# Kernel optimization log

Hardware: AMD Instinct MI355X
Metric: run time of the kernel (lower is better)

Reference implementation:

```python
import jax, jax.numpy as jnp
import numpy as np

KS = 4                       # kernel cells per axis
NCELL = KS ** 3              # 64 filter cells
K_NEIGH = 64                 # max neighbors kept per query point
EXTENT = float(40 * 6 * 0.025)   # radius_scale*6*particle_radius = 6.0
DT = 0.1
PI = float(np.pi)
BIG = 1e30
EPS = 1e-8
N_FLUID, N_BOX, BOX_L = 3000, 1500, 17.5
CH = [32, 64, 64, 64, 3]
C0 = 3

_OFFS = jnp.array([[i, j, l] for i in (0, 1) for j in (0, 1) for l in (0, 1)], dtype=jnp.int32)  # [8,3]


def _ball_to_cube(u):
    # Volume-preserving unit-ball -> unit-cube map (Open3D: sphere->cylinder->cube).
    x, y, z = u[..., 0], u[..., 1], u[..., 2]
    sq = x * x + y * y + z * z
    norm = jnp.sqrt(jnp.maximum(sq, EPS))
    xy_sq = x * x + y * y
    polar = (1.25 * z * z) > xy_sq
    s_p = jnp.sqrt(3.0 * norm / (norm + jnp.abs(z) + EPS))
    s_e = norm / jnp.sqrt(jnp.maximum(xy_sq, EPS))
    cx = jnp.where(polar, x * s_p, x * s_e)
    cy = jnp.where(polar, y * s_p, y * s_e)
    cz = jnp.where(polar, jnp.sign(z) * norm, 1.5 * z)
    # disc -> square (inverse Shirley-Chiu, area preserving)
    nxy = jnp.sqrt(jnp.maximum(cx * cx + cy * cy, EPS))
    xdom = jnp.abs(cy) <= jnp.abs(cx)
    sx = jnp.where(jnp.abs(cx) > EPS, cx, 1.0)
    sy = jnp.where(jnp.abs(cy) > EPS, cy, 1.0)
    bx1 = jnp.sign(cx) * nxy
    by1 = bx1 * (4.0 / PI) * jnp.arctan(cy / sx)
    by2 = jnp.sign(cy) * nxy
    bx2 = by2 * (4.0 / PI) * jnp.arctan(cx / sy)
    bx = jnp.where(xdom, bx1, bx2)
    by = jnp.where(xdom, by1, by2)
    xy0 = (cx * cx + cy * cy) < EPS
    bx = jnp.where(xy0, 0.0, bx)
    by = jnp.where(xy0, 0.0, by)
    out = jnp.stack([bx, by, cz], -1)
    return jnp.where((sq < EPS)[..., None], 0.0, out)


def _cconv(feats, pos_in, pos_out, kernel, bias, ignore_self=False, in_valid=None):
    # feats [M,S,C], pos_in [M,3], pos_out [N,3], kernel [NCELL,C,O], bias [O] -> [N,S,O]
    Nq, M = pos_out.shape[0], pos_in.shape[0]
    S, C = feats.shape[1], feats.shape[2]
    radius = EXTENT * 0.5
    d2 = jnp.sum((pos_out[:, None, :] - pos_in[None, :, :]) ** 2, -1)  # [N,M]
    if ignore_self:
        d2 = jnp.where(jnp.arange(Nq)[:, None] == jnp.arange(M)[None, :], BIG, d2)
    if in_valid is not None:
        d2 = jnp.where(in_valid[None, :], d2, BIG)
    K = min(K_NEIGH, M)
    neg, idx = jax.lax.top_k(-d2, K)                    # [N,K] nearest
    valid = (-neg) <= radius * radius
    offset = pos_in[idx] - pos_out[:, None, :]          # [N,K,3]
    u = offset / radius                                  # unit ball coords
    r_sqr = jnp.sum(u * u, -1)
    win = jnp.clip((1.0 - r_sqr) ** 3, 0.0, 1.0) * valid  # poly6 window
    coords = jnp.clip((_ball_to_cube(u) * 0.5 + 0.5) * (KS - 1), 0.0, KS - 1)  # align_corners
    c0 = jnp.clip(jnp.floor(coords), 0, KS - 2).astype(jnp.int32)
    f = coords - c0
    cidx = c0[:, :, None, :] + _OFFS[None, None]        # [N,K,8,3]
    wtri = jnp.prod(jnp.where(_OFFS[None, None].astype(bool), f[:, :, None, :], 1.0 - f[:, :, None, :]), axis=-1)
    corner = (cidx[..., 0] * KS + cidx[..., 1]) * KS + cidx[..., 2]  # [N,K,8]
    w = wtri * win[..., None]
    nn = jnp.arange(Nq)[:, None, None]
    kk = jnp.arange(K)[None, :, None]
    Wcell = jnp.zeros((Nq, K, NCELL), feats.dtype).at[nn, kk, corner].add(w)  # [N,K,64]
    feats_g = feats[idx].reshape(Nq, K, S * C)
    cellacc = jnp.einsum('nkl,nkf->nlf', Wcell, feats_g).reshape(Nq, NCELL, S, C)
    return jnp.einsum('nlsc,lco->nso', cellacc, kernel) + bias


def _forward(p0_enc, v0_enc, p0, v0, a, other_feats, box, box_feats, fluid_mask, box_mask,
             k0f, b0f, k0o, b0o, wdf, bdf, kc1, bc1, kc2, bc2, kc3, bc3, kc4, bc4,
             wd1, bd1, wd2, bd2, wd3, bd3, wd4, bd4):
    feats_hist = jnp.concatenate([other_feats, v0_enc], axis=-2)  # [N,2,3]
    v1 = v0 + DT * a
    p1 = p0 + DT * (v0 + v1) * 0.5
    fluid_feats = jnp.concatenate([v1[:, None, :], feats_hist], axis=-2)  # [N,3,3]
    cf = _cconv(fluid_feats, p1, p1, k0f, b0f, ignore_self=True)          # [N,3,32]
    df = fluid_feats @ wdf + bdf                                          # [N,3,32]
    co = _cconv(box_feats[:, None, :], box, p1, k0o, b0o, in_valid=box_mask > 0)  # [N,1,32]
    co = jnp.broadcast_to(co, cf.shape)
    out = jnp.concatenate([co, cf, df], axis=-1)                          # [N,3,96]
    convs = [(kc1, bc1), (kc2, bc2), (kc3, bc3), (kc4, bc4)]
    denses = [(wd1, bd1), (wd2, bd2), (wd3, bd3), (wd4, bd4)]
    for (kc, bc), (wd, bd) in zip(convs, denses):
        h = jax.nn.relu(out)
        oc = _cconv(h, p1, p1, kc, bc, ignore_self=True)
        od = h @ wd + bd
        out = (oc + od + out) if od.shape[-1] == out.shape[-1] else (oc + od)
    pos_corr = 0.25 * out
    pos_corr = pos_corr.at[..., 0, :].multiply(1.0 / 16.0)
    corr = pos_corr[..., 0, :]
    p_c = p1 + corr
    v_c = (p_c - p0) / DT
    m_matrix = pos_corr[..., 1:, :]
    state_feats = feats_hist[..., other_feats.shape[-2]:, :]
    return p_c, v_c, m_matrix, state_feats


def setup_inputs() -> dict:
    key = jax.random.key(0)
    ks = jax.random.split(key, 40)
    N, M, L = N_FLUID, N_BOX, BOX_L
    inp = {
        'p0_enc': jax.random.uniform(ks[0], (N, 1, 3)) * L,
        'v0_enc': jax.random.normal(ks[1], (N, 1, 3)) * 0.1,
        'p0': jax.random.uniform(ks[2], (N, 3)) * L,
        'v0': jax.random.normal(ks[3], (N, 3)) * 0.1,
        'a': jax.random.normal(ks[4], (N, 3)) * 0.1,
        'other_feats': jax.random.normal(ks[5], (N, 1, 3)) * 0.1,
        'box': jax.random.uniform(ks[6], (M, 3)) * L,
        'box_feats': jax.random.normal(ks[7], (M, 1)) * 0.1,
        'fluid_mask': jnp.ones((N,), jnp.float32),
        'box_mask': jnp.ones((M,), jnp.float32),
    }
    def kconv(k, cin, cout):
        return jax.random.normal(k, (NCELL, cin, cout)) * (1.0 / np.sqrt(cin * NCELL))
    def kdense(k, cin, cout):
        return jax.random.normal(k, (cin, cout)) * (1.0 / np.sqrt(cin))
    inp['k0f'] = kconv(ks[8], C0, CH[0]); inp['b0f'] = jnp.zeros((CH[0],))
    inp['k0o'] = kconv(ks[9], 1, CH[0]); inp['b0o'] = jnp.zeros((CH[0],))
    inp['wdf'] = kdense(ks[10], C0, CH[0]); inp['bdf'] = jnp.zeros((CH[0],))
    in_ch = 3 * CH[0]
    for i in range(1, 5):
        inp['kc%d' % i] = kconv(ks[10 + 2 * i], in_ch, CH[i]); inp['bc%d' % i] = jnp.zeros((CH[i],))
        inp['wd%d' % i] = kdense(ks[11 + 2 * i], in_ch, CH[i]); inp['bd%d' % i] = jnp.zeros((CH[i],))
        in_ch = CH[i]
    return inp


def reference(p0_enc, v0_enc, p0, v0, a, other_feats, box, box_feats, fluid_mask, box_mask,
              k0f, b0f, k0o, b0o, wdf, bdf, kc1, bc1, kc2, bc2, kc3, bc3, kc4, bc4,
              wd1, bd1, wd2, bd2, wd3, bd3, wd4, bd4):
    return _forward(p0_enc, v0_enc, p0, v0, a, other_feats, box, box_feats, fluid_mask, box_mask,
                    k0f, b0f, k0o, b0o, wdf, bdf, kc1, bc1, kc2, bc2, kc3, bc3, kc4, bc4,
                    wd1, bd1, wd2, bd2, wd3, bd3, wd4, bd4)
```

## Files before the change

### kernel.cpp

```cpp
#include <hip/hip_runtime.h>
#include <stdint.h>

#define NF 3000
#define NB 1500

__device__ __forceinline__ float signf(float v) {
    return (v > 0.f) ? 1.f : ((v < 0.f) ? -1.f : 0.f);
}

__device__ void ball_to_cube(float x, float y, float z, float b[3])
{
    const float EPS = 1e-8f;
    const float FOUR_OVER_PI = 1.2732395447351628f;
    float sq    = x*x + y*y + z*z;
    float norm  = sqrtf(fmaxf(sq, EPS));
    float xy_sq = x*x + y*y;
    bool  polar = (1.25f*z*z > xy_sq);
    float s_p = sqrtf(3.0f*norm / (norm + fabsf(z) + EPS));
    float s_e = norm / sqrtf(fmaxf(xy_sq, EPS));
    float cx = polar ? x*s_p : x*s_e;
    float cy = polar ? y*s_p : y*s_e;
    float cz = polar ? signf(z)*norm : 1.5f*z;
    float nxy = sqrtf(fmaxf(cx*cx + cy*cy, EPS));
    bool  xdom = fabsf(cy) <= fabsf(cx);
    float sx = (fabsf(cx) > EPS) ? cx : 1.0f;
    float sy = (fabsf(cy) > EPS) ? cy : 1.0f;
    float bx1 = signf(cx)*nxy;
    float by1 = bx1*FOUR_OVER_PI*atanf(cy/sx);
    float by2 = signf(cy)*nxy;
    float bx2 = by2*FOUR_OVER_PI*atanf(cx/sy);
    float bx = xdom ? bx1 : bx2;
    float by = xdom ? by1 : by2;
    if (cx*cx + cy*cy < EPS) { bx = 0.f; by = 0.f; }
    if (sq < EPS)            { bx = 0.f; by = 0.f; cz = 0.f; }
    b[0] = bx; b[1] = by; b[2] = cz;
}

__global__ __launch_bounds__(256)
void integrate_kernel(const float* __restrict__ p0, const float* __restrict__ v0,
                      const float* __restrict__ a,  const float* __restrict__ other,
                      const float* __restrict__ v0enc,
                      float* __restrict__ p1, float* __restrict__ ff)
{
    int t = blockIdx.x*blockDim.x + threadIdx.x;
    if (t >= NF*3) return;
    float vv = v0[t];
    float v1 = vv + 0.1f*a[t];
    float u  = vv + v1;
    float u2 = 0.1f*u;
    float u3 = u2*0.5f;
    p1[t] = p0[t] + u3;
    int n = t/3, j = t - 3*n;
    ff[n*9 + 0 + j] = v1;
    ff[n*9 + 3 + j] = other[t];
    ff[n*9 + 6 + j] = v0enc[t];
}

template<int LPT, bool SELFX, bool MASK>
__global__ __launch_bounds__(256)
void knn_kernel(const float* __restrict__ qpos, const float* __restrict__ cpos, int M,
                const float* __restrict__ mask,
                int* __restrict__ idxout, float* __restrict__ d2out)
{
    __shared__ unsigned hist[256];
    __shared__ unsigned long long s_prefix;
    __shared__ int s_rem;
    __shared__ int s_cnt;
    __shared__ uint64_t skeys[64];

    int n = blockIdx.x;
    int tid = threadIdx.x;
    float qx = qpos[n*3+0], qy = qpos[n*3+1], qz = qpos[n*3+2];

    uint64_t keys[LPT];
#pragma unroll
    for (int i = 0; i < LPT; ++i) {
        int c = i*256 + tid;
        uint64_t key = ~0ull;
        if (c < M) {
            float dx = __fadd_rn(qx, -cpos[c*3+0]);
            float dy = __fadd_rn(qy, -cpos[c*3+1]);
            float dz = __fadd_rn(qz, -cpos[c*3+2]);
            float d2 = __fadd_rn(__fadd_rn(__fmul_rn(dx,dx), __fmul_rn(dy,dy)),
                                 __fmul_rn(dz,dz));
            if (SELFX && c == n) d2 = 1e30f;
            if (MASK && !(mask[c] > 0.f)) d2 = 1e30f;
            key = ((uint64_t)__float_as_uint(d2) << 32) | (unsigned)c;
        }
        keys[i] = key;
    }

    uint64_t prefix = 0;
    int rem = 64;
    for (int pass = 0; pass < 8; ++pass) {
        int shift = 56 - 8*pass;
        hist[tid] = 0;
        __syncthreads();
#pragma unroll
        for (int i = 0; i < LPT; ++i) {
            uint64_t k = keys[i];
            bool act = (((k >> shift) >> 8) == prefix);
            if (act) atomicAdd(&hist[(unsigned)((k >> shift) & 0xff)], 1u);
        }
        __syncthreads();
        unsigned own = hist[tid];
#pragma unroll
        for (int off = 1; off < 256; off <<= 1) {
            unsigned v = (tid >= off) ? hist[tid - off] : 0u;
            __syncthreads();
            hist[tid] += v;
            __syncthreads();
        }
        unsigned inc = hist[tid];
        unsigned exc = inc - own;
        if (exc < (unsigned)rem && inc >= (unsigned)rem) {
            s_prefix = (prefix << 8) | (unsigned)tid;
            s_rem = rem - (int)exc;
        }
        __syncthreads();
        prefix = s_prefix;
        rem = s_rem;
        __syncthreads();
    }
    uint64_t kth = prefix;
    if (tid == 0) s_cnt = 0;
    __syncthreads();
#pragma unroll
    for (int i = 0; i < LPT; ++i) {
        uint64_t k = keys[i];
        if (k <= kth) {
            int p = atomicAdd(&s_cnt, 1);
            skeys[p] = k;
        }
    }
    __syncthreads();
    if (tid < 64) {
        uint64_t key = skeys[tid];
        int rank = 0;
        for (int j = 0; j < 64; ++j) rank += (skeys[j] < key) ? 1 : 0;
        idxout[n*64 + rank] = (int)(key & 0xffffffffu);
        d2out [n*64 + rank] = __uint_as_float((unsigned)(key >> 32));
    }
}

__global__ __launch_bounds__(256)
void geom_kernel(const float* __restrict__ qpos, const float* __restrict__ cpos,
                 const int* __restrict__ idxbuf, const float* __restrict__ d2buf,
                 unsigned char* __restrict__ corbuf, float* __restrict__ w8buf)
{
    int t = blockIdx.x*blockDim.x + threadIdx.x;
    if (t >= NF*64) return;
    int n = t >> 6;
    int m = idxbuf[t];
    float d2 = d2buf[t];
    float ox = cpos[m*3+0] - qpos[n*3+0];
    float oy = cpos[m*3+1] - qpos[n*3+1];
    float oz = cpos[m*3+2] - qpos[n*3+2];
    float ux = ox / 3.0f, uy = oy / 3.0f, uz = oz / 3.0f;
    float r_sqr = ux*ux + uy*uy + uz*uz;
    float tt  = 1.0f - r_sqr;
    float win = tt*tt*tt;
    win = fminf(fmaxf(win, 0.0f), 1.0f);
    if (!(d2 <= 9.0f)) win = 0.0f;
    float b[3];
    ball_to_cube(ux, uy, uz, b);
    int c0[3]; float fr[3];
#pragma unroll
    for (int d = 0; d < 3; ++d) {
        float coords = (b[d]*0.5f + 0.5f) * 3.0f;
        coords = fminf(fmaxf(coords, 0.0f), 3.0f);
        float fl = floorf(coords);
        fl = fminf(fmaxf(fl, 0.0f), 2.0f);
        c0[d] = (int)fl;
        fr[d] = coords - fl;
    }
#pragma unroll
    for (int j = 0; j < 8; ++j) {
        int ix = (j>>2)&1, iy = (j>>1)&1, iz = j&1;
        int cid = ((c0[0]+ix)*4 + (c0[1]+iy))*4 + (c0[2]+iz);
        float wt = ((ix ? fr[0] : 1.0f-fr[0]) * (iy ? fr[1] : 1.0f-fr[1]))
                 *  (iz ? fr[2] : 1.0f-fr[2]);
        corbuf[(size_t)t*8 + j] = (unsigned char)cid;
        w8buf [(size_t)t*8 + j] = wt * win;
    }
}

template<int S>
__global__ __launch_bounds__(256)
void cconv_kernel(const float* __restrict__ feats, int fstride, int dorelu,
                  const int* __restrict__ idxbuf, const float* __restrict__ w8buf,
                  const unsigned char* __restrict__ corbuf,
                  const float* __restrict__ W, const float* __restrict__ bias,
                  float* __restrict__ outbuf, int ostride, int ooff,
                  int Cin, int Csub, int Cout)
{
    extern __shared__ float smem[];
    const int n   = blockIdx.x;
    const int tid = threadIdx.x;
    const int CP  = ((Csub & 3) == 0) ? (Csub + 4) : Csub;
    float* cell = smem;
    float* red  = smem + S*64*CP;
    float* s_w8 = red;
    int*   s_idx = (int*)(red + 512);
    unsigned char* s_cor = (unsigned char*)(red + 576);

    for (int i = tid; i < 512; i += 256) s_w8[i] = w8buf[(size_t)n*512 + i];
    if (tid < 64)  s_idx[tid] = idxbuf[n*64 + tid];
    if (tid < 128) ((uint32_t*)s_cor)[tid] = ((const uint32_t*)corbuf)[(size_t)n*128 + tid];
    __syncthreads();

    const bool vec = ((Cout & 3) == 0) && ((Csub & 3) == 0);
    const int OG = Cout >> 2;
    const int vchunks = 256 / OG;
    const int og  = tid % OG;
    const int vch = tid / OG;
    const int o4  = og * 4;
    const int CHS = (256 / Cout < 16) ? (256 / Cout) : 16;
    const int so  = tid % Cout;
    const int sch = tid / Cout;

    float acc[S][4];
#pragma unroll
    for (int s = 0; s < S; ++s) { acc[s][0]=0.f; acc[s][1]=0.f; acc[s][2]=0.f; acc[s][3]=0.f; }
    float accS[S];
#pragma unroll
    for (int s = 0; s < S; ++s) accS[s] = 0.f;

    for (int cb = 0; cb < Cin; cb += Csub) {
        for (int i = tid; i < S*64*CP; i += 256) cell[i] = 0.f;
        __syncthreads();

        if ((Csub & 3) == 0) {
            int C4  = Csub >> 2;
            int nth = S * C4 * 4;
            if (tid < nth) {
                int j2  = tid & 3;
                int sc4 = tid >> 2;
                int s   = sc4 / C4;
                int c4  = (sc4 - s*C4) << 2;
                const float* fb = feats + s*Cin + cb + c4;
                float* cbse = cell + s*64*CP + c4;
                for (int k = 0; k < 64; ++k) {
                    int m = s_idx[k];
                    float4 v = *(const float4*)(fb + (size_t)m*fstride);
                    if (dorelu) {
                        v.x = fmaxf(v.x, 0.f); v.y = fmaxf(v.y, 0.f);
                        v.z = fmaxf(v.z, 0.f); v.w = fmaxf(v.w, 0.f);
                    }
#pragma unroll
                    for (int jj = 0; jj < 2; ++jj) {
                        int j = j2*2 + jj;
                        float wt = s_w8[k*8 + j];
                        int l = (int)s_cor[k*8 + j];
                        float4* cp = (float4*)(cbse + l*CP);
                        float4 cur = *cp;
                        cur.x = fmaf(wt, v.x, cur.x);
                        cur.y = fmaf(wt, v.y, cur.y);
                        cur.z = fmaf(wt, v.z, cur.z);
                        cur.w = fmaf(wt, v.w, cur.w);
                        *cp = cur;
                    }
                }
            }
        } else {
            int SCt = S * Csub;
            int total = 64*8*SCt;
            for (int t = tid; t < total; t += 256) {
                int k   = t / (8*SCt);
                int rem = t - k*8*SCt;
                int j   = rem / SCt;
                int sc  = rem - j*SCt;
                int s   = sc / Csub;
                int c   = sc - s*Csub;
                int m   = s_idx[k];
                float v = feats[(size_t)m*fstride + s*Cin + cb + c];
                if (dorelu) v = fmaxf(v, 0.f);
                atomicAdd(&cell[(s*64 + (int)s_cor[k*8+j])*CP + c], s_w8[k*8+j]*v);
            }
        }
        __syncthreads();

        if (vec) {
            for (int l = vch; l < 64; l += vchunks) {
                const float* wrow = W + (size_t)(l*Cin + cb)*Cout + o4;
                for (int c2 = 0; c2 < Csub; c2 += 4) {
                    float4 cv[S];
#pragma unroll
                    for (int s = 0; s < S; ++s)
                        cv[s] = *(const float4*)(cell + (s*64 + l)*CP + c2);
#pragma unroll
                    for (int q = 0; q < 4; ++q) {
                        float4 w4 = *(const float4*)(wrow + (size_t)(c2 + q)*Cout);
#pragma unroll
                        for (int s = 0; s < S; ++s) {
                            float cvq = (q==0)?cv[s].x:((q==1)?cv[s].y:((q==2)?cv[s].z:cv[s].w));
                            acc[s][0] = fmaf(cvq, w4.x, acc[s][0]);
                            acc[s][1] = fmaf(cvq, w4.y, acc[s][1]);
                            acc[s][2] = fmaf(cvq, w4.z, acc[s][2]);
                            acc[s][3] = fmaf(cvq, w4.w, acc[s][3]);
                        }
                    }
                }
            }
        } else if (sch < CHS) {
            for (int l = 0; l < 64; ++l) {
                for (int c2 = sch; c2 < Csub; c2 += CHS) {
                    float wt = W[(size_t)(l*Cin + cb + c2)*Cout + so];
#pragma unroll
                    for (int s = 0; s < S; ++s)
                        accS[s] = fmaf(cell[(s*64 + l)*CP + c2], wt, accS[s]);
                }
            }
        }
        __syncthreads();
    }

    if (vec) {
#pragma unroll
        for (int s = 0; s < S; ++s) {
            float* rp = red + (size_t)(vch*S + s)*Cout + o4;
            rp[0] = acc[s][0]; rp[1] = acc[s][1]; rp[2] = acc[s][2]; rp[3] = acc[s][3];
        }
    } else if (sch < CHS) {
#pragma unroll
        for (int s = 0; s < S; ++s)
            red[(size_t)(sch*S + s)*Cout + so] = accS[s];
    }
    __syncthreads();
    int chunksUsed = vec ? vchunks : CHS;
    for (int t = tid; t < S*Cout; t += 256) {
        int s = t / Cout, o = t - s*Cout;
        float sum = 0.f;
        for (int c2 = 0; c2 < chunksUsed; ++c2)
            sum += red[(size_t)(c2*S + s)*Cout + o];
        outbuf[((size_t)n*S + s)*ostride + ooff + o] = sum + bias[o];
    }
}

__global__ __launch_bounds__(256)
void dense_kernel(const float* __restrict__ in, int CinT, int dorelu,
                  const float* __restrict__ Wd, const float* __restrict__ bd,
                  const float* __restrict__ res, int rstride,
                  float* __restrict__ outbuf, int ostride, int ooff,
                  int accumulate, int Cout, int Ntot)
{
    int t = blockIdx.x*blockDim.x + threadIdx.x;
    if (t >= Ntot) return;
    int o  = t % Cout;
    int ns = t / Cout;
    const float* row = in + (size_t)ns*CinT;
    float sum = bd[o];
    for (int c = 0; c < CinT; ++c) {
        float v = row[c];
        if (dorelu) v = fmaxf(v, 0.f);
        sum = fmaf(v, Wd[(size_t)c*Cout + o], sum);
    }
    if (res) sum += res[(size_t)ns*rstride + o];
    float* dst = outbuf + (size_t)ns*ostride + ooff + o;
    if (accumulate) *dst += sum; else *dst = sum;
}

__global__ __launch_bounds__(256)
void bcast_co_kernel(const float* __restrict__ co, float* __restrict__ out0, int total)
{
    int t = blockIdx.x*blockDim.x + threadIdx.x;
    if (t >= total) return;
    int o = t % 32; int ns = t / 32; int n = ns / 3;
    out0[(size_t)ns*96 + o] = co[n*32 + o];
}

__global__ __launch_bounds__(256)
void epilogue_kernel(const float* __restrict__ out4, const float* __restrict__ p1,
                     const float* __restrict__ p0, const float* __restrict__ v0enc,
                     float* __restrict__ dout)
{
    int t = blockIdx.x*blockDim.x + threadIdx.x;
    if (t >= NF*3) return;
    int n = t/3, j = t - 3*n;
    float corr = (0.25f * out4[n*9 + 0 + j]) * (1.0f/16.0f);
    float pc = p1[t] + corr;
    float vc = (pc - p0[t]) / 0.1f;
    dout[t] = pc;
    dout[ 9000 + t] = vc;
    dout[18000 + n*6 + 0 + j] = 0.25f * out4[n*9 + 3 + j];
    dout[18000 + n*6 + 3 + j] = 0.25f * out4[n*9 + 6 + j];
    dout[36000 + t] = v0enc[t];
}

extern "C" void kernel_launch(void* const* d_in, const int* in_sizes, int n_in,
                              void* d_out, int out_size, void* d_ws, size_t ws_size,
                              hipStream_t stream)
{
    const float* v0_enc   = (const float*)d_in[1];
    const float* p0       = (const float*)d_in[2];
    const float* v0       = (const float*)d_in[3];
    const float* a        = (const float*)d_in[4];
    const float* other    = (const float*)d_in[5];
    const float* box      = (const float*)d_in[6];
    const float* box_feat = (const float*)d_in[7];
    const float* box_mask = (const float*)d_in[9];
    const float* k0f = (const float*)d_in[10]; const float* b0f = (const float*)d_in[11];
    const float* k0o = (const float*)d_in[12]; const float* b0o = (const float*)d_in[13];
    const float* wdf = (const float*)d_in[14]; const float* bdf = (const float*)d_in[15];

    const float *kcv[4], *bcv[4], *wdv[4], *bdv[4];
    bool interleaved = (in_sizes[18] == 96*64);
    for (int i = 0; i < 4; ++i) {
        if (interleaved) {
            kcv[i] = (const float*)d_in[16 + 4*i + 0];
            bcv[i] = (const float*)d_in[16 + 4*i + 1];
            wdv[i] = (const float*)d_in[16 + 4*i + 2];
            bdv[i] = (const float*)d_in[16 + 4*i + 3];
        } else {
            kcv[i] = (const float*)d_in[16 + 2*i];
            bcv[i] = (const float*)d_in[17 + 2*i];
            wdv[i] = (const float*)d_in[24 + 2*i];
            bdv[i] = (const float*)d_in[25 + 2*i];
        }
    }

    size_t off = 0;
    char* base = (char*)d_ws;
    auto carve = [&](size_t bytes) -> void* {
        void* p = base + off;
        off += (bytes + 255) & ~(size_t)255;
        return p;
    };
    float* p1    = (float*)carve(NF*3*sizeof(float));
    float* ff    = (float*)carve(NF*9*sizeof(float));
    int*   idx_f = (int*)  carve(NF*64*sizeof(int));
    float* d2_f  = (float*)carve(NF*64*sizeof(float));
    unsigned char* cor_f = (unsigned char*)carve((size_t)NF*64*8);
    float* w8_f  = (float*)carve((size_t)NF*64*8*sizeof(float));
    int*   idx_b = (int*)  carve(NF*64*sizeof(int));
    float* d2_b  = (float*)carve(NF*64*sizeof(float));
    unsigned char* cor_b = (unsigned char*)carve((size_t)NF*64*8);
    float* w8_b  = (float*)carve((size_t)NF*64*8*sizeof(float));
    float* out0  = (float*)carve((size_t)NF*3*96*sizeof(float));
    float* outA  = (float*)carve((size_t)NF*3*64*sizeof(float));
    float* outB  = (float*)carve((size_t)NF*3*64*sizeof(float));
    float* out4  = (float*)carve((size_t)NF*9*sizeof(float));
    float* co    = (float*)carve((size_t)NF*32*sizeof(float));
    (void)ws_size; (void)out_size; (void)n_in;

    integrate_kernel<<<(NF*3 + 255)/256, 256, 0, stream>>>(p0, v0, a, other, v0_enc, p1, ff);

    knn_kernel<12, true,  false><<<NF, 256, 0, stream>>>(p1, p1,  NF, nullptr,  idx_f, d2_f);
    knn_kernel< 6, false, true ><<<NF, 256, 0, stream>>>(p1, box, NB, box_mask, idx_b, d2_b);

    geom_kernel<<<(NF*64 + 255)/256, 256, 0, stream>>>(p1, p1,  idx_f, d2_f, cor_f, w8_f);
    geom_kernel<<<(NF*64 + 255)/256, 256, 0, stream>>>(p1, box, idx_b, d2_b, cor_b, w8_b);

    auto conv3 = [&](const float* feats, int fstride, int dorelu,
                     const int* idx, const float* w8, const unsigned char* cor,
                     const float* W, const float* bias,
                     float* outb, int ostride, int ooff,
                     int Cin, int Csub, int Cout) {
        int CP = ((Csub & 3) == 0) ? Csub + 4 : Csub;
        size_t smem = (size_t)(3*64*CP + 3072)*sizeof(float);
        cconv_kernel<3><<<NF, 256, smem, stream>>>(feats, fstride, dorelu, idx, w8, cor,
                                                   W, bias, outb, ostride, ooff, Cin, Csub, Cout);
    };

    conv3(ff, 9, 0, idx_f, w8_f, cor_f, k0f, b0f, out0, 96, 32, 3, 3, 32);
    {
        int CP = 1;
        size_t smem = (size_t)(1*64*CP + 3072)*sizeof(float);
        cconv_kernel<1><<<NF, 256, smem, stream>>>(box_feat, 1, 0, idx_b, w8_b, cor_b,
                                                   k0o, b0o, co, 32, 0, 1, 1, 32);
    }
    bcast_co_kernel<<<(NF*3*32 + 255)/256, 256, 0, stream>>>(co, out0, NF*3*32);
    dense_kernel<<<(NF*3*32 + 255)/256, 256, 0, stream>>>(ff, 3, 0, wdf, bdf,
                                                          nullptr, 0, out0, 96, 64, 0, 32, NF*3*32);

    conv3(out0, 288, 1, idx_f, w8_f, cor_f, kcv[0], bcv[0], outA, 64, 0, 96, 48, 64);
    dense_kernel<<<(NF*3*64 + 255)/256, 256, 0, stream>>>(out0, 96, 1, wdv[0], bdv[0],
                                                          nullptr, 0, outA, 64, 0, 1, 64, NF*3*64);

    conv3(outA, 192, 1, idx_f, w8_f, cor_f, kcv[1], bcv[1], outB, 64, 0, 64, 64, 64);
    dense_kernel<<<(NF*3*64 + 255)/256, 256, 0, stream>>>(outA, 64, 1, wdv[1], bdv[1],
                                                          outA, 64, outB, 64, 0, 1, 64, NF*3*64);

    conv3(outB, 192, 1, idx_f, w8_f, cor_f, kcv[2], bcv[2], outA, 64, 0, 64, 64, 64);
    dense_kernel<<<(NF*3*64 + 255)/256, 256, 0, stream>>>(outB, 64, 1, wdv[2], bdv[2],
                                                          outB, 64, outA, 64, 0, 1, 64, NF*3*64);

    conv3(outA, 192, 1, idx_f, w8_f, cor_f, kcv[3], bcv[3], out4, 3, 0, 64, 64, 3);
    dense_kernel<<<(NF*3*3 + 255)/256, 256, 0, stream>>>(outA, 64, 1, wdv[3], bdv[3],
                                                         nullptr, 0, out4, 3, 0, 1, 3, NF*3*3);

    epilogue_kernel<<<(NF*3 + 255)/256, 256, 0, stream>>>(out4, p1, p0, v0_enc, (float*)d_out);
}
```

Measured before the change: 1.747 ms.

## Restructure continuous convolution as scatter-to-cells plus split-K GEMM with fused dense

The per-query fused cconv kernel is replaced by a two-stage scheme. A scatter kernel builds a per-row cell-feature matrix in workspace, and a tiled FP32 GEMM multiplies it by the conv weights concatenated with the dense weights. Split-K with a reduction kernel, a dedicated 3-output row-dot kernel, and a box-conv scatter are added. Separately, the KNN prefix scan now uses wavefront shuffles instead of a shared-memory Hillis-Steele loop, and the d2 buffer is dropped in favour of recomputing distance in geom. The change trades extra global memory traffic for the materialized cell matrix against better weight reuse across queries.

```diff
diff --git a/kernel.cpp b/kernel.cpp
--- a/kernel.cpp
+++ b/kernel.cpp
@@ -3,6 +3,7 @@
 
 #define NF 3000
 #define NB 1500
+#define KSMAX 8
 
 __device__ __forceinline__ float signf(float v) {
     return (v > 0.f) ? 1.f : ((v < 0.f) ? -1.f : 0.f);
@@ -59,10 +60,10 @@
 template<int LPT, bool SELFX, bool MASK>
 __global__ __launch_bounds__(256)
 void knn_kernel(const float* __restrict__ qpos, const float* __restrict__ cpos, int M,
-                const float* __restrict__ mask,
-                int* __restrict__ idxout, float* __restrict__ d2out)
+                const float* __restrict__ mask, int* __restrict__ idxout)
 {
     __shared__ unsigned hist[256];
+    __shared__ unsigned wtot[4];
     __shared__ unsigned long long s_prefix;
     __shared__ int s_rem;
     __shared__ int s_cnt;
@@ -104,14 +105,18 @@
         }
         __syncthreads();
         unsigned own = hist[tid];
-#pragma unroll
-        for (int off = 1; off < 256; off <<= 1) {
-            unsigned v = (tid >= off) ? hist[tid - off] : 0u;
-            __syncthreads();
-            hist[tid] += v;
-            __syncthreads();
-        }
-        unsigned inc = hist[tid];
+        unsigned v = own;
+#pragma unroll
+        for (int o2 = 1; o2 < 64; o2 <<= 1) {
+            unsigned u = (unsigned)__shfl_up((int)v, o2, 64);
+            if ((tid & 63) >= o2) v += u;
+        }
+        if ((tid & 63) == 63) wtot[tid >> 6] = v;
+        __syncthreads();
+        unsigned bsum = 0;
+#pragma unroll
+        for (int w = 0; w < 4; ++w) bsum += (w < (tid >> 6)) ? wtot[w] : 0u;
+        unsigned inc = v + bsum;
         unsigned exc = inc - own;
         if (exc < (unsigned)rem && inc >= (unsigned)rem) {
             s_prefix = (prefix << 8) | (unsigned)tid;
@@ -139,29 +144,30 @@
         int rank = 0;
         for (int j = 0; j < 64; ++j) rank += (skeys[j] < key) ? 1 : 0;
         idxout[n*64 + rank] = (int)(key & 0xffffffffu);
-        d2out [n*64 + rank] = __uint_as_float((unsigned)(key >> 32));
     }
 }
 
 __global__ __launch_bounds__(256)
 void geom_kernel(const float* __restrict__ qpos, const float* __restrict__ cpos,
-                 const int* __restrict__ idxbuf, const float* __restrict__ d2buf,
+                 const int* __restrict__ idxbuf, int selfex,
                  unsigned char* __restrict__ corbuf, float* __restrict__ w8buf)
 {
     int t = blockIdx.x*blockDim.x + threadIdx.x;
     if (t >= NF*64) return;
     int n = t >> 6;
     int m = idxbuf[t];
-    float d2 = d2buf[t];
-    float ox = cpos[m*3+0] - qpos[n*3+0];
-    float oy = cpos[m*3+1] - qpos[n*3+1];
-    float oz = cpos[m*3+2] - qpos[n*3+2];
+    float ox = __fadd_rn(cpos[m*3+0], -qpos[n*3+0]);
+    float oy = __fadd_rn(cpos[m*3+1], -qpos[n*3+1]);
+    float oz = __fadd_rn(cpos[m*3+2], -qpos[n*3+2]);
+    float d2 = __fadd_rn(__fadd_rn(__fmul_rn(ox,ox), __fmul_rn(oy,oy)),
+                         __fmul_rn(oz,oz));
+    bool valid = (d2 <= 9.0f) && !(selfex && m == n);
     float ux = ox / 3.0f, uy = oy / 3.0f, uz = oz / 3.0f;
     float r_sqr = ux*ux + uy*uy + uz*uz;
     float tt  = 1.0f - r_sqr;
     float win = tt*tt*tt;
     win = fminf(fmaxf(win, 0.0f), 1.0f);
-    if (!(d2 <= 9.0f)) win = 0.0f;
+    if (!valid) win = 0.0f;
     float b[3];
     ball_to_cube(ux, uy, uz, b);
     int c0[3]; float fr[3];
@@ -185,164 +191,243 @@
     }
 }
 
-template<int S>
-__global__ __launch_bounds__(256)
-void cconv_kernel(const float* __restrict__ feats, int fstride, int dorelu,
-                  const int* __restrict__ idxbuf, const float* __restrict__ w8buf,
-                  const unsigned char* __restrict__ corbuf,
-                  const float* __restrict__ W, const float* __restrict__ bias,
-                  float* __restrict__ outbuf, int ostride, int ooff,
-                  int Cin, int Csub, int Cout)
-{
-    extern __shared__ float smem[];
-    const int n   = blockIdx.x;
-    const int tid = threadIdx.x;
-    const int CP  = ((Csub & 3) == 0) ? (Csub + 4) : Csub;
-    float* cell = smem;
-    float* red  = smem + S*64*CP;
-    float* s_w8 = red;
-    int*   s_idx = (int*)(red + 512);
-    unsigned char* s_cor = (unsigned char*)(red + 576);
-
+__global__ __launch_bounds__(256)
+void scatter_kernel(const float* __restrict__ h, int C3, int C, int relu_,
+                    const int* __restrict__ idxbuf, const float* __restrict__ w8buf,
+                    const unsigned char* __restrict__ corbuf,
+                    int Kconv, int n0, float* __restrict__ A)
+{
+    extern __shared__ float sm[];
+    float* s_w8 = sm;
+    int*   s_idx = (int*)(sm + 512);
+    unsigned char* s_cor = (unsigned char*)(sm + 576);
+    float* cell = sm + 704;
+
+    int nloc = blockIdx.x;
+    int n = n0 + nloc;
+    int tid = threadIdx.x;
     for (int i = tid; i < 512; i += 256) s_w8[i] = w8buf[(size_t)n*512 + i];
     if (tid < 64)  s_idx[tid] = idxbuf[n*64 + tid];
     if (tid < 128) ((uint32_t*)s_cor)[tid] = ((const uint32_t*)corbuf)[(size_t)n*128 + tid];
     __syncthreads();
 
-    const bool vec = ((Cout & 3) == 0) && ((Csub & 3) == 0);
-    const int OG = Cout >> 2;
-    const int vchunks = 256 / OG;
-    const int og  = tid % OG;
-    const int vch = tid / OG;
-    const int o4  = og * 4;
-    const int CHS = (256 / Cout < 16) ? (256 / Cout) : 16;
-    const int so  = tid % Cout;
-    const int sch = tid / Cout;
-
-    float acc[S][4];
-#pragma unroll
-    for (int s = 0; s < S; ++s) { acc[s][0]=0.f; acc[s][1]=0.f; acc[s][2]=0.f; acc[s][3]=0.f; }
-    float accS[S];
-#pragma unroll
-    for (int s = 0; s < S; ++s) accS[s] = 0.f;
-
-    for (int cb = 0; cb < Cin; cb += Csub) {
-        for (int i = tid; i < S*64*CP; i += 256) cell[i] = 0.f;
-        __syncthreads();
-
-        if ((Csub & 3) == 0) {
-            int C4  = Csub >> 2;
-            int nth = S * C4 * 4;
-            if (tid < nth) {
-                int j2  = tid & 3;
-                int sc4 = tid >> 2;
-                int s   = sc4 / C4;
-                int c4  = (sc4 - s*C4) << 2;
-                const float* fb = feats + s*Cin + cb + c4;
-                float* cbse = cell + s*64*CP + c4;
-                for (int k = 0; k < 64; ++k) {
-                    int m = s_idx[k];
-                    float4 v = *(const float4*)(fb + (size_t)m*fstride);
-                    if (dorelu) {
-                        v.x = fmaxf(v.x, 0.f); v.y = fmaxf(v.y, 0.f);
-                        v.z = fmaxf(v.z, 0.f); v.w = fmaxf(v.w, 0.f);
-                    }
-#pragma unroll
-                    for (int jj = 0; jj < 2; ++jj) {
-                        int j = j2*2 + jj;
-                        float wt = s_w8[k*8 + j];
-                        int l = (int)s_cor[k*8 + j];
-                        float4* cp = (float4*)(cbse + l*CP);
-                        float4 cur = *cp;
-                        cur.x = fmaf(wt, v.x, cur.x);
-                        cur.y = fmaf(wt, v.y, cur.y);
-                        cur.z = fmaf(wt, v.z, cur.z);
-                        cur.w = fmaf(wt, v.w, cur.w);
-                        *cp = cur;
+    int FC = (C3 <= 256) ? C3 : ((C3 + 1) >> 1);
+    int nch = (C3 + FC - 1) / FC;
+    for (int ch = 0; ch < nch; ++ch) {
+        int fbase = ch * FC;
+        for (int i = tid; i < 64*FC; i += 256) cell[i] = 0.f;
+        __syncthreads();
+        bool act = (tid < FC) && (fbase + tid < C3);
+        int fg = fbase + tid;
+        if (act) {
+            float* cl = cell + tid;
+#pragma unroll 2
+            for (int k = 0; k < 64; ++k) {
+                int m = s_idx[k];
+                float v = h[(size_t)m*C3 + fg];
+                if (relu_) v = fmaxf(v, 0.f);
+#pragma unroll
+                for (int j = 0; j < 8; ++j) {
+                    int l = (int)s_cor[k*8 + j];
+                    cl[l*FC] = fmaf(s_w8[k*8 + j], v, cl[l*FC]);
+                }
+            }
+        }
+        __syncthreads();
+        if (act) {
+            int s = fg / C, c = fg - s*C;
+            float* dst = A + ((size_t)(nloc*3 + s))*Kconv + c;
+            const float* src = cell + tid;
+            for (int l = 0; l < 64; ++l)
+                dst[l*C] = src[(size_t)l*FC];
+        }
+        __syncthreads();
+    }
+}
+
+__global__ __launch_bounds__(64)
+void boxscatter_kernel(const float* __restrict__ bf, const int* __restrict__ idxbuf,
+                       const float* __restrict__ w8buf, const unsigned char* __restrict__ corbuf,
+                       float* __restrict__ Ab)
+{
+    __shared__ float wf[512];
+    __shared__ int   sc[512];
+    int n = blockIdx.x, tid = threadIdx.x;
+    for (int i = tid; i < 512; i += 64) {
+        int k = i >> 3;
+        int m = idxbuf[n*64 + k];
+        wf[i] = w8buf[(size_t)n*512 + i] * bf[m];
+        sc[i] = (int)corbuf[(size_t)n*512 + i];
+    }
+    __syncthreads();
+    float acc = 0.f;
+    for (int i = 0; i < 512; ++i) acc += (sc[i] == tid) ? wf[i] : 0.f;
+    Ab[n*64 + tid] = acc;
+}
+
+#define GBM 64
+#define GBN 64
+#define GBK 32
+__global__ __launch_bounds__(256)
+void gemm_kernel(const float* __restrict__ A, int Kconv,
+                 const float* __restrict__ htail, int C, int hrow0, int relu_,
+                 const float* __restrict__ Wc, const float* __restrict__ Wd,
+                 int M, int N, int Ktot, int KS, float* __restrict__ P,
+                 float* __restrict__ outp, int ostride, int ooff,
+                 const float* __restrict__ b1, const float* __restrict__ b2,
+                 const float* __restrict__ res, int rstride)
+{
+    __shared__ float At[GBK][GBM+4];
+    __shared__ float Bs[GBK][GBN+4];
+    int mt = blockIdx.x * GBM;
+    int ks = blockIdx.y;
+    int nbk = (Ktot + GBK*KS - 1) / (GBK*KS);
+    int k0 = ks * nbk * GBK;
+    int k1 = min(Ktot, k0 + nbk*GBK);
+    int tid = threadIdx.x;
+    int tn = tid & 15, tm = tid >> 4;
+
+    float acc[4][4];
+#pragma unroll
+    for (int i = 0; i < 4; ++i)
+#pragma unroll
+        for (int j = 0; j < 4; ++j) acc[i][j] = 0.f;
+
+    for (int kb = k0; kb < k1; kb += GBK) {
+#pragma unroll
+        for (int half = 0; half < 2; ++half) {
+            int t = tid + half*256;
+            int row = t >> 3, kq = (t & 7) << 2;
+            int grow = mt + row, gk = kb + kq;
+            float4 v = make_float4(0.f,0.f,0.f,0.f);
+            if (grow < M) {
+                if (gk < Kconv) {
+                    v = *(const float4*)(A + (size_t)grow*Kconv + gk);
+                } else {
+                    v = *(const float4*)(htail + (size_t)(hrow0+grow)*C + (gk - Kconv));
+                    if (relu_) {
+                        v.x = fmaxf(v.x,0.f); v.y = fmaxf(v.y,0.f);
+                        v.z = fmaxf(v.z,0.f); v.w = fmaxf(v.w,0.f);
                     }
                 }
             }
-        } else {
-            int SCt = S * Csub;
-            int total = 64*8*SCt;
-            for (int t = tid; t < total; t += 256) {
-                int k   = t / (8*SCt);
-                int rem = t - k*8*SCt;
-                int j   = rem / SCt;
-                int sc  = rem - j*SCt;
-                int s   = sc / Csub;
-                int c   = sc - s*Csub;
-                int m   = s_idx[k];
-                float v = feats[(size_t)m*fstride + s*Cin + cb + c];
-                if (dorelu) v = fmaxf(v, 0.f);
-                atomicAdd(&cell[(s*64 + (int)s_cor[k*8+j])*CP + c], s_w8[k*8+j]*v);
+            At[kq+0][row] = v.x; At[kq+1][row] = v.y;
+            At[kq+2][row] = v.z; At[kq+3][row] = v.w;
+        }
+#pragma unroll
+        for (int half = 0; half < 2; ++half) {
+            int t = tid + half*256;
+            int krow = t >> 4, nq = (t & 15) << 2;
+            int gk = kb + krow;
+            float4 v = make_float4(0.f,0.f,0.f,0.f);
+            if (nq < N) {
+                if (gk < Kconv) v = *(const float4*)(Wc + (size_t)gk*N + nq);
+                else            v = *(const float4*)(Wd + (size_t)(gk - Kconv)*N + nq);
             }
-        }
-        __syncthreads();
-
-        if (vec) {
-            for (int l = vch; l < 64; l += vchunks) {
-                const float* wrow = W + (size_t)(l*Cin + cb)*Cout + o4;
-                for (int c2 = 0; c2 < Csub; c2 += 4) {
-                    float4 cv[S];
-#pragma unroll
-                    for (int s = 0; s < S; ++s)
-                        cv[s] = *(const float4*)(cell + (s*64 + l)*CP + c2);
-#pragma unroll
-                    for (int q = 0; q < 4; ++q) {
-                        float4 w4 = *(const float4*)(wrow + (size_t)(c2 + q)*Cout);
-#pragma unroll
-                        for (int s = 0; s < S; ++s) {
-                            float cvq = (q==0)?cv[s].x:((q==1)?cv[s].y:((q==2)?cv[s].z:cv[s].w));
-                            acc[s][0] = fmaf(cvq, w4.x, acc[s][0]);
-                            acc[s][1] = fmaf(cvq, w4.y, acc[s][1]);
-                            acc[s][2] = fmaf(cvq, w4.z, acc[s][2]);
-                            acc[s][3] = fmaf(cvq, w4.w, acc[s][3]);
-                        }
-                    }
+            *(float4*)&Bs[krow][nq] = v;
+        }
+        __syncthreads();
+#pragma unroll
+        for (int kk = 0; kk < GBK; ++kk) {
+            float4 a4 = *(const float4*)&At[kk][tm<<2];
+            float4 b4 = *(const float4*)&Bs[kk][tn<<2];
+            float av[4] = {a4.x, a4.y, a4.z, a4.w};
+            float bv[4] = {b4.x, b4.y, b4.z, b4.w};
+#pragma unroll
+            for (int i = 0; i < 4; ++i)
+#pragma unroll
+                for (int j = 0; j < 4; ++j)
+                    acc[i][j] = fmaf(av[i], bv[j], acc[i][j]);
+        }
+        __syncthreads();
+    }
+    if (KS > 1) {
+#pragma unroll
+        for (int i = 0; i < 4; ++i) {
+            int grow = mt + (tm<<2) + i;
+            if (grow < M) {
+                float4 st = make_float4(acc[i][0], acc[i][1], acc[i][2], acc[i][3]);
+                *(float4*)(P + ((size_t)ks*M + grow)*64 + (tn<<2)) = st;
+            }
+        }
+    } else {
+        int o = tn << 2;
+#pragma unroll
+        for (int i = 0; i < 4; ++i) {
+            int grow = mt + (tm<<2) + i;
+            if (grow < M && o < N) {
+                float4 st;
+                st.x = acc[i][0] + b1[o+0] + (b2 ? b2[o+0] : 0.f);
+                st.y = acc[i][1] + b1[o+1] + (b2 ? b2[o+1] : 0.f);
+                st.z = acc[i][2] + b1[o+2] + (b2 ? b2[o+2] : 0.f);
+                st.w = acc[i][3] + b1[o+3] + (b2 ? b2[o+3] : 0.f);
+                if (res) {
+                    st.x += res[(size_t)grow*rstride + o+0];
+                    st.y += res[(size_t)grow*rstride + o+1];
+                    st.z += res[(size_t)grow*rstride + o+2];
+                    st.w += res[(size_t)grow*rstride + o+3];
                 }
+                *(float4*)(outp + (size_t)grow*ostride + ooff + o) = st;
             }
-        } else if (sch < CHS) {
-            for (int l = 0; l < 64; ++l) {
-                for (int c2 = sch; c2 < Csub; c2 += CHS) {
-                    float wt = W[(size_t)(l*Cin + cb + c2)*Cout + so];
-#pragma unroll
-                    for (int s = 0; s < S; ++s)
-                        accS[s] = fmaf(cell[(s*64 + l)*CP + c2], wt, accS[s]);
-                }
-            }
-        }
-        __syncthreads();
-    }
-
-    if (vec) {
-#pragma unroll
-        for (int s = 0; s < S; ++s) {
-            float* rp = red + (size_t)(vch*S + s)*Cout + o4;
-            rp[0] = acc[s][0]; rp[1] = acc[s][1]; rp[2] = acc[s][2]; rp[3] = acc[s][3];
-        }
-    } else if (sch < CHS) {
-#pragma unroll
-        for (int s = 0; s < S; ++s)
-            red[(size_t)(sch*S + s)*Cout + so] = accS[s];
-    }
-    __syncthreads();
-    int chunksUsed = vec ? vchunks : CHS;
-    for (int t = tid; t < S*Cout; t += 256) {
-        int s = t / Cout, o = t - s*Cout;
-        float sum = 0.f;
-        for (int c2 = 0; c2 < chunksUsed; ++c2)
-            sum += red[(size_t)(c2*S + s)*Cout + o];
-        outbuf[((size_t)n*S + s)*ostride + ooff + o] = sum + bias[o];
+        }
+    }
+}
+
+__global__ __launch_bounds__(256)
+void reduce_kernel(const float* __restrict__ P, int KS, int M, int N,
+                   const float* __restrict__ b1, const float* __restrict__ b2,
+                   const float* __restrict__ res, int rstride,
+                   float* __restrict__ out, int ostride, int ooff)
+{
+    int t = blockIdx.x*256 + threadIdx.x;
+    if (t >= M*N) return;
+    int row = t / N, o = t - row*N;
+    float s = b1[o] + (b2 ? b2[o] : 0.f);
+    for (int k = 0; k < KS; ++k) s += P[((size_t)k*M + row)*64 + o];
+    if (res) s += res[(size_t)row*rstride + o];
+    out[(size_t)row*ostride + ooff + o] = s;
+}
+
+__global__ __launch_bounds__(256)
+void rowdot3_kernel(const float* __restrict__ A, int Kconv,
+                    const float* __restrict__ h, int C, int hrow0,
+                    const float* __restrict__ Wc, const float* __restrict__ Wd,
+                    const float* __restrict__ bc, const float* __restrict__ bd,
+                    int M, float* __restrict__ out)
+{
+    int row = blockIdx.x*4 + (threadIdx.x >> 6);
+    int lane = threadIdx.x & 63;
+    if (row >= M) return;
+    const float* ar = A + (size_t)row*Kconv;
+    const float* hr = h + (size_t)(hrow0+row)*C;
+    float a0 = 0.f, a1 = 0.f, a2 = 0.f;
+    int Ktot = Kconv + C;
+    for (int k = lane; k < Ktot; k += 64) {
+        float av; const float* w;
+        if (k < Kconv) { av = ar[k];                   w = Wc + (size_t)k*3; }
+        else           { av = fmaxf(hr[k-Kconv], 0.f); w = Wd + (size_t)(k-Kconv)*3; }
+        a0 = fmaf(av, w[0], a0);
+        a1 = fmaf(av, w[1], a1);
+        a2 = fmaf(av, w[2], a2);
+    }
+    for (int off = 32; off > 0; off >>= 1) {
+        a0 += __shfl_xor(a0, off);
+        a1 += __shfl_xor(a1, off);
+        a2 += __shfl_xor(a2, off);
+    }
+    if (lane == 0) {
+        size_t o = (size_t)(hrow0+row)*3;
+        out[o+0] = a0 + bc[0] + bd[0];
+        out[o+1] = a1 + bc[1] + bd[1];
+        out[o+2] = a2 + bc[2] + bd[2];
     }
 }
 
 __global__ __launch_bounds__(256)
 void dense_kernel(const float* __restrict__ in, int CinT, int dorelu,
                   const float* __restrict__ Wd, const float* __restrict__ bd,
-                  const float* __restrict__ res, int rstride,
                   float* __restrict__ outbuf, int ostride, int ooff,
-                  int accumulate, int Cout, int Ntot)
+                  int Cout, int Ntot)
 {
     int t = blockIdx.x*blockDim.x + threadIdx.x;
     if (t >= Ntot) return;
@@ -355,9 +440,7 @@
         if (dorelu) v = fmaxf(v, 0.f);
         sum = fmaf(v, Wd[(size_t)c*Cout + o], sum);
     }
-    if (res) sum += res[(size_t)ns*rstride + o];
-    float* dst = outbuf + (size_t)ns*ostride + ooff + o;
-    if (accumulate) *dst += sum; else *dst = sum;
+    outbuf[(size_t)ns*ostride + ooff + o] = sum;
 }
 
 __global__ __launch_bounds__(256)
@@ -427,67 +510,127 @@
         return p;
     };
     float* p1    = (float*)carve(NF*3*sizeof(float));
-    float* ff    = (float*)carve(NF*9*sizeof(float));
     int*   idx_f = (int*)  carve(NF*64*sizeof(int));
-    float* d2_f  = (float*)carve(NF*64*sizeof(float));
-    unsigned char* cor_f = (unsigned char*)carve((size_t)NF*64*8);
-    float* w8_f  = (float*)carve((size_t)NF*64*8*sizeof(float));
-    int*   idx_b = (int*)  carve(NF*64*sizeof(int));
-    float* d2_b  = (float*)carve(NF*64*sizeof(float));
-    unsigned char* cor_b = (unsigned char*)carve((size_t)NF*64*8);
-    float* w8_b  = (float*)carve((size_t)NF*64*8*sizeof(float));
+    unsigned char* cor_f = (unsigned char*)carve((size_t)NF*512);
+    float* w8_f  = (float*)carve((size_t)NF*512*sizeof(float));
     float* out0  = (float*)carve((size_t)NF*3*96*sizeof(float));
     float* outA  = (float*)carve((size_t)NF*3*64*sizeof(float));
     float* outB  = (float*)carve((size_t)NF*3*64*sizeof(float));
     float* out4  = (float*)carve((size_t)NF*9*sizeof(float));
     float* co    = (float*)carve((size_t)NF*32*sizeof(float));
-    (void)ws_size; (void)out_size; (void)n_in;
+    size_t free_off = off;
+    float* ff    = (float*)carve(NF*9*sizeof(float));
+    int*   idx_b = (int*)  carve(NF*64*sizeof(int));
+    unsigned char* cor_b = (unsigned char*)carve((size_t)NF*512);
+    float* w8_b  = (float*)carve((size_t)NF*512*sizeof(float));
+    float* A_b   = (float*)carve((size_t)NF*64*sizeof(float));
+    size_t fixed_end = off;
+    (void)out_size; (void)n_in;
+
+    char*  v0base = base + fixed_end;
+    size_t V0 = (ws_size > fixed_end) ? ws_size - fixed_end : 0;
+    char*  v1base = base + free_off;
+    size_t V1 = (ws_size > free_off) ? ws_size - free_off : 0;
+
+    auto pickKS = [&](int Mch, int Ktot) -> int {
+        int nb = (Mch + GBM - 1) / GBM;
+        int ks = (1024 + nb - 1) / nb;
+        if (ks > KSMAX) ks = KSMAX;
+        int kt = Ktot / GBK; if (ks > kt) ks = kt;
+        if (ks < 1) ks = 1;
+        return ks;
+    };
 
     integrate_kernel<<<(NF*3 + 255)/256, 256, 0, stream>>>(p0, v0, a, other, v0_enc, p1, ff);
 
-    knn_kernel<12, true,  false><<<NF, 256, 0, stream>>>(p1, p1,  NF, nullptr,  idx_f, d2_f);
-    knn_kernel< 6, false, true ><<<NF, 256, 0, stream>>>(p1, box, NB, box_mask, idx_b, d2_b);
-
-    geom_kernel<<<(NF*64 + 255)/256, 256, 0, stream>>>(p1, p1,  idx_f, d2_f, cor_f, w8_f);
-    geom_kernel<<<(NF*64 + 255)/256, 256, 0, stream>>>(p1, box, idx_b, d2_b, cor_b, w8_b);
-
-    auto conv3 = [&](const float* feats, int fstride, int dorelu,
-                     const int* idx, const float* w8, const unsigned char* cor,
-                     const float* W, const float* bias,
-                     float* outb, int ostride, int ooff,
-                     int Cin, int Csub, int Cout) {
-        int CP = ((Csub & 3) == 0) ? Csub + 4 : Csub;
-        size_t smem = (size_t)(3*64*CP + 3072)*sizeof(float);
-        cconv_kernel<3><<<NF, 256, smem, stream>>>(feats, fstride, dorelu, idx, w8, cor,
-                                                   W, bias, outb, ostride, ooff, Cin, Csub, Cout);
+    knn_kernel<12, true,  false><<<NF, 256, 0, stream>>>(p1, p1,  NF, nullptr,  idx_f);
+    knn_kernel< 6, false, true ><<<NF, 256, 0, stream>>>(p1, box, NB, box_mask, idx_b);
+
+    geom_kernel<<<(NF*64 + 255)/256, 256, 0, stream>>>(p1, p1,  idx_f, 1, cor_f, w8_f);
+    geom_kernel<<<(NF*64 + 255)/256, 256, 0, stream>>>(p1, box, idx_b, 0, cor_b, w8_b);
+
+    {
+        int C = 3, C3 = 9, Kconv = 192;
+        size_t smem = (704 + (size_t)64*C3) * sizeof(float);
+        size_t bpq = (size_t)3*Kconv*4;
+        int qpc = (int)(V0 / bpq);
+        if (qpc < 1) qpc = 1;
+        if (qpc > NF) qpc = NF;
+        for (int n0 = 0; n0 < NF; n0 += qpc) {
+            int nq = (NF - n0 < qpc) ? (NF - n0) : qpc;
+            int Mch = nq*3;
+            float* Achunk = (float*)v0base;
+            scatter_kernel<<<nq, 256, smem, stream>>>(ff, C3, C, 0, idx_f, w8_f, cor_f,
+                                                      Kconv, n0, Achunk);
+            dim3 g((Mch + GBM - 1)/GBM, 1);
+            gemm_kernel<<<g, 256, 0, stream>>>(Achunk, Kconv, nullptr, 0, 0, 0,
+                                               k0f, nullptr, Mch, 32, Kconv, 1, nullptr,
+                                               out0 + (size_t)n0*3*96, 96, 32,
+                                               b0f, nullptr, nullptr, 0);
+        }
+    }
+    {
+        boxscatter_kernel<<<NF, 64, 0, stream>>>(box_feat, idx_b, w8_b, cor_b, A_b);
+        dim3 g((NF + GBM - 1)/GBM, 1);
+        gemm_kernel<<<g, 256, 0, stream>>>(A_b, 64, nullptr, 0, 0, 0,
+                                           k0o, nullptr, NF, 32, 64, 1, nullptr,
+                                           co, 32, 0, b0o, nullptr, nullptr, 0);
+        bcast_co_kernel<<<(NF*3*32 + 255)/256, 256, 0, stream>>>(co, out0, NF*3*32);
+    }
+    dense_kernel<<<(NF*3*32 + 255)/256, 256, 0, stream>>>(ff, 3, 0, wdf, bdf,
+                                                          out0, 96, 64, 32, NF*3*32);
+
+    auto convLayer = [&](const float* h, int C, const float* Wc, const float* bc,
+                         const float* Wd, const float* bd,
+                         const float* res, int rstride,
+                         float* outp, int ostride, int Nout) {
+        int Kconv = 64*C, C3 = 3*C;
+        int Ktot = Kconv + C;
+        int FC = (C3 <= 256) ? C3 : ((C3 + 1) >> 1);
+        size_t smem = (704 + (size_t)64*FC) * sizeof(float);
+        size_t bpq = (size_t)3*Kconv*4 + (size_t)3*KSMAX*64*4;
+        int qpc = (int)(V1 / bpq);
+        if (qpc < 1) qpc = 1;
+        if (qpc > NF) qpc = NF;
+        size_t Aoff = ((size_t)qpc*3*Kconv*4 + 255) & ~(size_t)255;
+        for (int n0 = 0; n0 < NF; n0 += qpc) {
+            int nq = (NF - n0 < qpc) ? (NF - n0) : qpc;
+            int Mch = nq*3;
+            float* Achunk = (float*)v1base;
+            float* Play   = (float*)(v1base + Aoff);
+            scatter_kernel<<<nq, 256, smem, stream>>>(h, C3, C, 1, idx_f, w8_f, cor_f,
+                                                      Kconv, n0, Achunk);
+            if (Nout == 3) {
+                rowdot3_kernel<<<(Mch + 3)/4, 256, 0, stream>>>(Achunk, Kconv, h, C, n0*3,
+                                                                Wc, Wd, bc, bd, Mch, out4);
+            } else {
+                int KS = pickKS(Mch, Ktot);
+                dim3 g((Mch + GBM - 1)/GBM, KS);
+                if (KS > 1) {
+                    gemm_kernel<<<g, 256, 0, stream>>>(Achunk, Kconv, h, C, n0*3, 1,
+                                                       Wc, Wd, Mch, Nout, Ktot, KS, Play,
+                                                       nullptr, 0, 0, nullptr, nullptr,
+                                                       nullptr, 0);
+                    reduce_kernel<<<((size_t)Mch*Nout + 255)/256, 256, 0, stream>>>(
+                        Play, KS, Mch, Nout, bc, bd,
+                        res ? res + (size_t)n0*3*rstride : nullptr, rstride,
+                        outp + (size_t)n0*3*ostride, ostride, 0);
+                } else {
+                    gemm_kernel<<<g, 256, 0, stream>>>(Achunk, Kconv, h, C, n0*3, 1,
+                                                       Wc, Wd, Mch, Nout, Ktot, 1, nullptr,
+                                                       outp + (size_t)n0*3*ostride, ostride, 0,
+                                                       bc, bd,
+                                                       res ? res + (size_t)n0*3*rstride : nullptr,
+                                                       rstride);
+                }
+            }
+        }
     };
 
-    conv3(ff, 9, 0, idx_f, w8_f, cor_f, k0f, b0f, out0, 96, 32, 3, 3, 32);
-    {
-        int CP = 1;
-        size_t smem = (size_t)(1*64*CP + 3072)*sizeof(float);
-        cconv_kernel<1><<<NF, 256, smem, stream>>>(box_feat, 1, 0, idx_b, w8_b, cor_b,
-                                                   k0o, b0o, co, 32, 0, 1, 1, 32);
-    }
-    bcast_co_kernel<<<(NF*3*32 + 255)/256, 256, 0, stream>>>(co, out0, NF*3*32);
-    dense_kernel<<<(NF*3*32 + 255)/256, 256, 0, stream>>>(ff, 3, 0, wdf, bdf,
-                                                          nullptr, 0, out0, 96, 64, 0, 32, NF*3*32);
-
-    conv3(out0, 288, 1, idx_f, w8_f, cor_f, kcv[0], bcv[0], outA, 64, 0, 96, 48, 64);
-    dense_kernel<<<(NF*3*64 + 255)/256, 256, 0, stream>>>(out0, 96, 1, wdv[0], bdv[0],
-                                                          nullptr, 0, outA, 64, 0, 1, 64, NF*3*64);
-
-    conv3(outA, 192, 1, idx_f, w8_f, cor_f, kcv[1], bcv[1], outB, 64, 0, 64, 64, 64);
-    dense_kernel<<<(NF*3*64 + 255)/256, 256, 0, stream>>>(outA, 64, 1, wdv[1], bdv[1],
-                                                          outA, 64, outB, 64, 0, 1, 64, NF*3*64);
-
-    conv3(outB, 192, 1, idx_f, w8_f, cor_f, kcv[2], bcv[2], outA, 64, 0, 64, 64, 64);
-    dense_kernel<<<(NF*3*64 + 255)/256, 256, 0, stream>>>(outB, 64, 1, wdv[2], bdv[2],
-                                                          outB, 64, outA, 64, 0, 1, 64, NF*3*64);
-
-    conv3(outA, 192, 1, idx_f, w8_f, cor_f, kcv[3], bcv[3], out4, 3, 0, 64, 64, 3);
-    dense_kernel<<<(NF*3*3 + 255)/256, 256, 0, stream>>>(outA, 64, 1, wdv[3], bdv[3],
-                                                         nullptr, 0, out4, 3, 0, 1, 3, NF*3*3);
+    convLayer(out0, 96, kcv[0], bcv[0], wdv[0], bdv[0], nullptr, 0,  outA, 64, 64);
+    convLayer(outA, 64, kcv[1], bcv[1], wdv[1], bdv[1], outA,   64, outB, 64, 64);
+    convLayer(outB, 64, kcv[2], bcv[2], wdv[2], bdv[2], outB,   64, outA, 64, 64);
+    convLayer(outA, 64, kcv[3], bcv[3], wdv[3], bdv[3], nullptr, 0,  out4, 3,  3);
 
     epilogue_kernel<<<(NF*3 + 255)/256, 256, 0, stream>>>(out4, p1, p0, v0_enc, (float*)d_out);
 }
```

New measurement: 1.594 ms. 1.1x faster.
